# Kernel optimization log

Measured on AMD Instinct MI355X. Metric: run time of the kernel, lower is better.

## Reference

```python
import jax, jax.numpy as jnp
import numpy as np

B, L, D = 16, 1024, 1024
OUT_LEN = 24
N_LAYERS = 3
CYCLE = L
LN_EPS = 1e-5


def _make_pe(seq_len, hidden, cycle):
    # pe[t, j] = 2*pi*t/cycle, then sin on even cols, cos on odd cols
    t = jnp.arange(seq_len, dtype=jnp.float32)[:, None]
    base = (2.0 * jnp.pi * t / cycle) * jnp.ones((1, hidden), jnp.float32)
    cols = jnp.arange(hidden)
    return jnp.where((cols % 2 == 0)[None, :], jnp.sin(base), jnp.cos(base))


def setup_inputs() -> dict:
    key = jax.random.key(0)
    ks = jax.random.split(key, 12)
    s = 0.02
    return {
        "x": jax.random.normal(ks[0], (B, L, D), jnp.float32),
        "pe": _make_pe(L, D, CYCLE),
        "w1": jax.random.normal(ks[1], (N_LAYERS, D, D), jnp.float32) * s,
        "b1": jnp.zeros((N_LAYERS, D), jnp.float32),
        "w2": jax.random.normal(ks[2], (N_LAYERS, D, D), jnp.float32) * s,
        "b2": jnp.zeros((N_LAYERS, D), jnp.float32),
        "ln_g": jnp.ones((N_LAYERS, D), jnp.float32),
        "ln_b": jnp.zeros((N_LAYERS, D), jnp.float32),
        "fc_w": jax.random.normal(ks[3], (1, D), jnp.float32) * s,
        "fc_b": jnp.zeros((1,), jnp.float32),
        "final_w": jax.random.normal(ks[4], (OUT_LEN, L), jnp.float32) * s,
        "final_b": jnp.zeros((OUT_LEN,), jnp.float32),
    }


def _layer_norm(y, g, b):
    mu = jnp.mean(y, axis=-1, keepdims=True)
    var = jnp.mean((y - mu) ** 2, axis=-1, keepdims=True)
    return (y - mu) * jax.lax.rsqrt(var + LN_EPS) * g + b


def reference(x, pe, w1, b1, w2, b2, ln_g, ln_b, fc_w, fc_b, final_w, final_b):
    d = x.shape[-1]
    scale = 1.0 / jnp.sqrt(jnp.float32(d))
    # positional add (pe[:, :seq_len]; here L == D so this is the full buffer)
    h = x + pe[:, : x.shape[1]]
    attns = []
    for l in range(w1.shape[0]):
        # hand-rolled bmm-softmax-bmm self-attention (q = k = v = h)
        scores = jnp.einsum("bqd,bkd->bqk", h, h) * scale  # (B, L, L)
        a = jax.nn.softmax(scores, axis=-1)
        ctx = jnp.einsum("bqk,bkd->bqd", a, h)
        # position-wise FFN with hidden == D, residual over ctx, then LN
        ff = jnp.maximum(ctx @ w1[l].T + b1[l], 0.0) @ w2[l].T + b2[l]
        h = _layer_norm(ctx + ff, ln_g[l], ln_b[l])
        attns.append(a)
    # final head: D -> 1, squeeze, then L -> OUT_LEN over the sequence dim
    z = (h @ fc_w.T + fc_b)[..., 0]  # (B, L)
    out = z @ final_w.T + final_b    # (B, OUT_LEN)
    return (out, jnp.stack(attns))
```

## Files before the change

kernel.cpp:

```cpp
#include <hip/hip_runtime.h>

typedef unsigned short u16;
typedef __attribute__((ext_vector_type(8))) short short8;
typedef __attribute__((ext_vector_type(4))) float f32x4;
typedef __attribute__((ext_vector_type(4))) unsigned short u16x4;

__device__ __forceinline__ float bf2f(u16 u){
  union { unsigned int i; float f; } x; x.i = ((unsigned int)u) << 16; return x.f;
}
__device__ __forceinline__ u16 f2bf(float f){
  union { float f; unsigned int i; } x; x.f = f;
  return (u16)((x.i + 0x7fffu + ((x.i >> 16) & 1u)) >> 16);
}
__device__ __forceinline__ void async16(const void* g, void* s){
  __builtin_amdgcn_global_load_lds((const __attribute__((address_space(1))) void*)g,
                                   (__attribute__((address_space(3))) void*)s, 16, 0, 0);
}

__global__ __launch_bounds__(256) void k_split2(const float* __restrict__ s1, u16* __restrict__ d1,
                                                const float* __restrict__ s2, u16* __restrict__ d2){
  long i = ((long)blockIdx.x * 256 + threadIdx.x) * 4;
  f32x4 v1 = *(const f32x4*)(s1 + i);
  f32x4 v2 = *(const f32x4*)(s2 + i);
  u16x4 h1, h2;
  #pragma unroll
  for (int j=0;j<4;j++){ h1[j] = f2bf(v1[j]); h2[j] = f2bf(v2[j]); }
  *(u16x4*)(d1+i) = h1;
  *(u16x4*)(d2+i) = h2;
}

__global__ __launch_bounds__(256) void k_addpe(const float* __restrict__ x, const float* __restrict__ pe,
                                               u16* __restrict__ d){
  long i = ((long)blockIdx.x * 256 + threadIdx.x) * 4;
  f32x4 xv = *(const f32x4*)(x + i);
  f32x4 pv = *(const f32x4*)(pe + (i & 1048575));
  u16x4 hh;
  #pragma unroll
  for (int j=0;j<4;j++) hh[j] = f2bf(xv[j]+pv[j]);
  *(u16x4*)(d+i) = hh;
}

__global__ __launch_bounds__(256) void k_transpose(const u16* __restrict__ in, u16* __restrict__ outp){
  __shared__ u16 tile[64][68];
  const long b = blockIdx.z;
  const int d0 = blockIdx.x * 64, l0 = blockIdx.y * 64;
  const long ibase = b * 1048576l;
  const int t = threadIdx.x;
  const int cr = t >> 4;
  const int cc = (t & 15) * 4;
  #pragma unroll
  for (int rr=0; rr<4; rr++){
    int row = cr + rr*16;
    u16x4 v = *(const u16x4*)(in + ibase + (long)(l0+row)*1024 + d0 + cc);
    *(u16x4*)&tile[row][cc] = v;
  }
  __syncthreads();
  #pragma unroll
  for (int rr=0; rr<4; rr++){
    int drow = cr + rr*16;
    u16x4 y;
    y[0] = tile[cc+0][drow];
    y[1] = tile[cc+1][drow];
    y[2] = tile[cc+2][drow];
    y[3] = tile[cc+3][drow];
    *(u16x4*)(outp + ibase + (long)(d0+drow)*1024 + l0 + cc) = y;
  }
}

__global__ __launch_bounds__(512, 1) void attn_sm(
    const u16* __restrict__ hB, float* __restrict__ probs, u16* __restrict__ pB)
{
  __shared__ __align__(16) u16 sm[65536];
  const int t = threadIdx.x;
  const int w = t >> 6, lane = t & 63;
  const int fr = lane & 15, fs = lane >> 4;

  const int p = blockIdx.x;
  const int id = (p & 7) * 32 + (p >> 3);
  const long bz = id >> 4;
  const int brow = (id & 15) << 6;

  const u16* hb = hB + bz * 1048576l;

  const u16* gsrc[8];
  int gdst[8];
  #pragma unroll
  for (int c=0;c<8;c++){
    int u = c*512 + t;
    int row = u >> 2;
    int slot = (u & 3) ^ ((row >> 1) & 3);
    gsrc[c] = hb + (long)row*1024 + slot*8;
    gdst[c] = c*4096 + w*512;
  }

  int offA[4], offB[8];
  #pragma unroll
  for (int i=0;i<4;i++){
    int x = i*16 + fr;
    offA[i] = (brow + x)*32 + (fs ^ (((brow + x)>>1)&3))*8;
  }
  #pragma unroll
  for (int j=0;j<8;j++){
    int x = w*128 + j*16 + fr;
    offB[j] = x*32 + (fs ^ ((x>>1)&3))*8;
  }

  f32x4 acc[4][8];
  #pragma unroll
  for (int i=0;i<4;i++)
    #pragma unroll
    for (int j=0;j<8;j++) acc[i][j] = (f32x4){0.f,0.f,0.f,0.f};

  #pragma unroll
  for (int c=0;c<8;c++) async16(gsrc[c], sm + gdst[c]);
  asm volatile("s_waitcnt vmcnt(0)" ::: "memory");
  __builtin_amdgcn_s_barrier();
  __builtin_amdgcn_sched_barrier(0);

#define ATT_BODY(BUF)                                                          \
    short8 aF[4], bF[8];                                                       \
    _Pragma("unroll")                                                          \
    for (int i=0;i<4;i++) aF[i] = *(const short8*)((BUF) + offA[i]);           \
    _Pragma("unroll")                                                          \
    for (int j=0;j<8;j++) bF[j] = *(const short8*)((BUF) + offB[j]);           \
    __builtin_amdgcn_s_setprio(1);                                             \
    _Pragma("unroll")                                                          \
    for (int i=0;i<4;i++)                                                      \
      _Pragma("unroll")                                                        \
      for (int j=0;j<8;j++)                                                    \
        acc[i][j] = __builtin_amdgcn_mfma_f32_16x16x32_bf16(aF[i], bF[j], acc[i][j], 0,0,0); \
    __builtin_amdgcn_s_setprio(0);

  for (int kt = 0; kt < 31; ++kt){
    const u16* buf = sm + (kt & 1)*32768;
    u16* stg = sm + ((kt + 1) & 1)*32768;
    const int ko = (kt + 1)*32;
    #pragma unroll
    for (int c=0;c<8;c++) async16(gsrc[c] + ko, stg + gdst[c]);
    ATT_BODY(buf)
    asm volatile("s_waitcnt vmcnt(0)" ::: "memory");
    __builtin_amdgcn_s_barrier();
    __builtin_amdgcn_sched_barrier(0);
  }
  {
    const u16* buf = sm + 32768;
    ATT_BODY(buf)
  }
#undef ATT_BODY

  float* red = (float*)sm;
  const float SC = 0.03125f;

  float mx[4][4];
  #pragma unroll
  for (int i=0;i<4;i++)
    #pragma unroll
    for (int q=0;q<4;q++){
      float m = acc[i][0][q];
      #pragma unroll
      for (int j=1;j<8;j++) m = fmaxf(m, acc[i][j][q]);
      #pragma unroll
      for (int d=1; d<16; d<<=1) m = fmaxf(m, __shfl_xor(m, d));
      mx[i][q] = m;
    }
  if (fr == 0){
    #pragma unroll
    for (int i=0;i<4;i++)
      #pragma unroll
      for (int q=0;q<4;q++) red[(i*16 + fs*4 + q)*8 + w] = mx[i][q];
  }
  __syncthreads();
  float M[4][4];
  #pragma unroll
  for (int i=0;i<4;i++)
    #pragma unroll
    for (int q=0;q<4;q++){
      const int row = i*16 + fs*4 + q;
      f32x4 a = *(const f32x4*)&red[row*8];
      f32x4 b = *(const f32x4*)&red[row*8+4];
      M[i][q] = fmaxf(fmaxf(fmaxf(a[0],a[1]),fmaxf(a[2],a[3])),
                      fmaxf(fmaxf(b[0],b[1]),fmaxf(b[2],b[3])));
    }
  float sum[4][4];
  #pragma unroll
  for (int i=0;i<4;i++)
    #pragma unroll
    for (int q=0;q<4;q++){
      float s = 0.f;
      #pragma unroll
      for (int j=0;j<8;j++){
        float e = expf((acc[i][j][q] - M[i][q]) * SC);
        acc[i][j][q] = e;
        s += e;
      }
      #pragma unroll
      for (int d=1; d<16; d<<=1) s += __shfl_xor(s, d);
      sum[i][q] = s;
    }
  __syncthreads();
  if (fr == 0){
    #pragma unroll
    for (int i=0;i<4;i++)
      #pragma unroll
      for (int q=0;q<4;q++) red[(i*16 + fs*4 + q)*8 + w] = sum[i][q];
  }
  __syncthreads();
  float inv[4][4];
  #pragma unroll
  for (int i=0;i<4;i++)
    #pragma unroll
    for (int q=0;q<4;q++){
      const int row = i*16 + fs*4 + q;
      f32x4 a = *(const f32x4*)&red[row*8];
      f32x4 b = *(const f32x4*)&red[row*8+4];
      inv[i][q] = 1.0f / (a[0]+a[1]+a[2]+a[3]+b[0]+b[1]+b[2]+b[3]);
    }

  const long obase = bz * 1048576l;
  #pragma unroll
  for (int i=0;i<4;i++)
    #pragma unroll
    for (int q=0;q<4;q++){
      const long rbase = obase + (long)(brow + i*16 + fs*4 + q)*1024;
      const float iv = inv[i][q];
      #pragma unroll
      for (int j=0;j<8;j++){
        const int col = w*128 + j*16 + fr;
        const float pv = acc[i][j][q] * iv;
        probs[rbase + col] = pv;
        pB[rbase + col] = f2bf(pv);
      }
    }
}

template<int MODE>
__global__ __launch_bounds__(512, 2) void gemm8(
    const u16* __restrict__ aB, const u16* __restrict__ bB,
    int per, long sA, long sB, long sC,
    int lda, int ldb, int ldc,
    float scale, const float* __restrict__ bias,
    const u16* __restrict__ res,
    float* __restrict__ cF, u16* __restrict__ cB)
{
  __shared__ __align__(16) u16 sm[65536];
  const int t = threadIdx.x;
  const int w = t >> 6, lane = t & 63;
  const int wm = w >> 2, wn = w & 3;
  const int fr = lane & 15, fs = lane >> 4;

  const int p = blockIdx.x;
  const int chunk = gridDim.x >> 3;
  const int id = (p & 7) * chunk + (p >> 3);
  const long bz = id / per;
  const int rem = id % per;
  const int m0 = (rem >> 2) << 8, n0 = (rem & 3) << 8;

  const u16* a = aB + bz * sA;
  const u16* b = bB + bz * sB;

  const int urow = t >> 2;
  const int col8 = ((t & 3) ^ ((t >> 3) & 3)) * 8;
  const u16* gA0 = a + (long)(m0 + urow) * lda + col8;
  const u16* gA1 = a + (long)(m0 + 128 + urow) * lda + col8;
  const u16* gB0 = b + (long)(n0 + urow) * ldb + col8;
  const u16* gB1 = b + (long)(n0 + 128 + urow) * ldb + col8;
  u16* dA0 = sm + (w << 9);
  u16* dA1 = sm + 4096 + (w << 9);
  u16* dB0 = sm + 8192 + (w << 9);
  u16* dB1 = sm + 12288 + (w << 9);

  int offA[8], offB[4];
  #pragma unroll
  for (int i=0;i<8;i++){
    int row = wm*128 + i*16 + fr;
    int sl = fs ^ ((row >> 1) & 3);
    offA[i] = row*32 + sl*8;
  }
  #pragma unroll
  for (int j=0;j<4;j++){
    int row = wn*64 + j*16 + fr;
    int sl = fs ^ ((row >> 1) & 3);
    offB[j] = 8192 + row*32 + sl*8;
  }

  f32x4 acc[8][4];
  #pragma unroll
  for (int i=0;i<8;i++)
    #pragma unroll
    for (int j=0;j<4;j++) acc[i][j] = (f32x4){0.f,0.f,0.f,0.f};

  #pragma unroll
  for (int pb=0; pb<3; ++pb){
    const int kb = pb*32, sb = pb*16384;
    async16(gA0+kb, dA0+sb); async16(gA1+kb, dA1+sb);
    async16(gB0+kb, dB0+sb); async16(gB1+kb, dB1+sb);
  }
  gA0 += 96; gA1 += 96; gB0 += 96; gB1 += 96;
  asm volatile("s_waitcnt vmcnt(8)" ::: "memory");
  __builtin_amdgcn_s_barrier();
  __builtin_amdgcn_sched_barrier(0);

#define KT_BODY(SMB)                                                           \
    short8 aF[8], bF[4];                                                       \
    _Pragma("unroll")                                                          \
    for (int i=0;i<8;i++) aF[i] = *(const short8*)((SMB) + offA[i]);           \
    _Pragma("unroll")                                                          \
    for (int j=0;j<4;j++) bF[j] = *(const short8*)((SMB) + offB[j]);           \
    __builtin_amdgcn_s_barrier();                                              \
    __builtin_amdgcn_sched_barrier(0);                                         \
    __builtin_amdgcn_s_setprio(1);                                             \
    _Pragma("unroll")                                                          \
    for (int i=0;i<8;i++){                                                     \
      acc[i][0] = __builtin_amdgcn_mfma_f32_16x16x32_bf16(aF[i], bF[0], acc[i][0], 0,0,0); \
      acc[i][1] = __builtin_amdgcn_mfma_f32_16x16x32_bf16(aF[i], bF[1], acc[i][1], 0,0,0); \
    }                                                                          \
    _Pragma("unroll")                                                          \
    for (int i=0;i<8;i++){                                                     \
      acc[i][2] = __builtin_amdgcn_mfma_f32_16x16x32_bf16(aF[i], bF[2], acc[i][2], 0,0,0); \
      acc[i][3] = __builtin_amdgcn_mfma_f32_16x16x32_bf16(aF[i], bF[3], acc[i][3], 0,0,0); \
    }                                                                          \
    __builtin_amdgcn_s_setprio(0);

  for (int kt = 0; kt < 29; ++kt){
    const u16* smb = sm + (kt & 3)*16384;
    const int sb = ((kt + 3) & 3)*16384;
    async16(gA0, dA0+sb); async16(gA1, dA1+sb);
    async16(gB0, dB0+sb); async16(gB1, dB1+sb);
    gA0 += 32; gA1 += 32; gB0 += 32; gB1 += 32;
    KT_BODY(smb)
    asm volatile("s_waitcnt vmcnt(8)" ::: "memory");
    __builtin_amdgcn_s_barrier();
    __builtin_amdgcn_sched_barrier(0);
  }
  {
    const u16* smb = sm + (29 & 3)*16384;
    KT_BODY(smb)
    asm volatile("s_waitcnt vmcnt(4)" ::: "memory");
    __builtin_amdgcn_s_barrier();
    __builtin_amdgcn_sched_barrier(0);
  }
  {
    const u16* smb = sm + (30 & 3)*16384;
    KT_BODY(smb)
    asm volatile("s_waitcnt vmcnt(0)" ::: "memory");
    __builtin_amdgcn_s_barrier();
    __builtin_amdgcn_sched_barrier(0);
  }
  {
    const u16* smb = sm + (31 & 3)*16384;
    KT_BODY(smb)
  }
#undef KT_BODY

  const long cBase = bz * sC;
  const int rb = m0 + wm*128 + fs*4;
  const int cb = n0 + wn*64 + fr;
  #pragma unroll
  for (int j=0;j<4;j++){
    const int c = cb + j*16;
    float bv = 0.f;
    if constexpr (MODE == 2 || MODE == 3) bv = bias[c];
    #pragma unroll
    for (int i=0;i<8;i++){
      #pragma unroll
      for (int q=0;q<4;q++){
        const int r = rb + i*16 + q;
        const long idx = cBase + (long)r*ldc + c;
        float v = acc[i][j][q];
        if constexpr (MODE == 1){
          cB[idx] = f2bf(v);
        } else if constexpr (MODE == 2){
          cB[idx] = f2bf(fmaxf(v + bv, 0.f));
        } else {
          cF[idx] = v + bv + bf2f(res[idx]);
        }
      }
    }
  }
}

__global__ __launch_bounds__(256) void k_ln(const float* __restrict__ r,
                                            const float* __restrict__ g, const float* __restrict__ b,
                                            u16* __restrict__ h){
  const long row = blockIdx.x;
  const float* rr = r + row * 1024;
  const int t = threadIdx.x, w = t >> 6, lane = t & 63;
  __shared__ float rA[4], rB[4];
  f32x4 v = *(const f32x4*)(rr + t*4);
  float s = v[0]+v[1]+v[2]+v[3];
  #pragma unroll
  for (int off=32; off; off>>=1) s += __shfl_xor(s, off);
  if (lane==0) rA[w] = s;
  __syncthreads();
  const float mu = (rA[0]+rA[1]+rA[2]+rA[3]) * (1.0f/1024.0f);
  float sq = 0.f;
  #pragma unroll
  for (int j=0;j<4;j++){ float d = v[j]-mu; sq += d*d; }
  #pragma unroll
  for (int off=32; off; off>>=1) sq += __shfl_xor(sq, off);
  if (lane==0) rB[w] = sq;
  __syncthreads();
  const float var = (rB[0]+rB[1]+rB[2]+rB[3]) * (1.0f/1024.0f);
  const float inv = rsqrtf(var + 1e-5f);
  u16x4 hh;
  #pragma unroll
  for (int j=0;j<4;j++){
    int d = t*4+j;
    hh[j] = f2bf((v[j]-mu)*inv*g[d] + b[d]);
  }
  *(u16x4*)(h + row*1024 + t*4) = hh;
}

__global__ __launch_bounds__(256) void k_final1(const u16* __restrict__ h,
                                                const float* __restrict__ fw, const float* __restrict__ fb,
                                                float* __restrict__ z){
  const int row = blockIdx.x*4 + (threadIdx.x>>6);
  const int lane = threadIdx.x & 63;
  const long base = (long)row * 1024;
  const int d0 = lane * 16;
  float s = 0.f;
  #pragma unroll
  for (int j=0;j<16;j++){
    int d = d0 + j;
    s += bf2f(h[base+d]) * fw[d];
  }
  #pragma unroll
  for (int off=32; off; off>>=1) s += __shfl_xor(s, off);
  if (lane==0) z[row] = s + fb[0];
}

__global__ __launch_bounds__(256) void k_final2(const float* __restrict__ z,
                                                const float* __restrict__ fw, const float* __restrict__ fb,
                                                float* __restrict__ out){
  const int idx = blockIdx.x*4 + (threadIdx.x>>6);
  const int lane = threadIdx.x & 63;
  const int b = idx / 24, o = idx % 24;
  float s = 0.f;
  #pragma unroll
  for (int j=0;j<16;j++){
    int li = lane + j*64;
    s += z[b*1024 + li] * fw[o*1024 + li];
  }
  #pragma unroll
  for (int off=32; off; off>>=1) s += __shfl_xor(s, off);
  if (lane==0) out[idx] = s + fb[o];
}

extern "C" void kernel_launch(void* const* d_in, const int* in_sizes, int n_in,
                              void* d_out, int out_size, void* d_ws, size_t ws_size,
                              hipStream_t stream){
  const float* x   = (const float*)d_in[0];
  const float* pe  = (const float*)d_in[1];
  const float* w1  = (const float*)d_in[2];
  const float* b1  = (const float*)d_in[3];
  const float* w2  = (const float*)d_in[4];
  const float* b2  = (const float*)d_in[5];
  const float* lng = (const float*)d_in[6];
  const float* lnb = (const float*)d_in[7];
  const float* fcw = (const float*)d_in[8];
  const float* fcb = (const float*)d_in[9];
  const float* fw  = (const float*)d_in[10];
  const float* fb  = (const float*)d_in[11];
  float* out  = (float*)d_out;
  float* attn = out + 384;

  char* ws = (char*)d_ws;
  const long BB = 32l*1024*1024;
  u16* hB = (u16*)(ws + 0*BB);
  u16* tB = (u16*)(ws + 1*BB);
  u16* cB = (u16*)(ws + 2*BB);
  u16* pB = (u16*)(ws + 3*BB);
  float* rf = (float*)(ws + 4*BB);
  u16* w1B = (u16*)(ws + 6*BB);
  u16* w2B = w1B + 3l*1024*1024;
  float* z = (float*)(w2B + 3l*1024*1024);

  const long M1 = 1024l*1024;

  k_split2<<<3072, 256, 0, stream>>>(w1, w1B, w2, w2B);
  k_addpe<<<16384, 256, 0, stream>>>(x, pe, hB);
  k_transpose<<<dim3(16,16,16), 256, 0, stream>>>(hB, tB);

  for (int l = 0; l < 3; l++){
    float* sc = attn + (long)l*16*M1;
    attn_sm<<<256, 512, 0, stream>>>(hB, sc, pB);
    gemm8<1><<<256, 512, 0, stream>>>(pB, tB, 16, M1,M1,M1, 1024,1024,1024,
        1.f, nullptr, nullptr, nullptr, cB);
    gemm8<2><<<256, 512, 0, stream>>>(cB, w1B+l*M1, 256, 0,0,0, 1024,1024,1024,
        1.f, b1+l*1024, nullptr, nullptr, pB);
    gemm8<3><<<256, 512, 0, stream>>>(pB, w2B+l*M1, 256, 0,0,0, 1024,1024,1024,
        1.f, b2+l*1024, cB, rf, nullptr);
    k_ln<<<16384, 256, 0, stream>>>(rf, lng+l*1024, lnb+l*1024, hB);
    if (l < 2) k_transpose<<<dim3(16,16,16), 256, 0, stream>>>(hB, tB);
  }

  k_final1<<<4096, 256, 0, stream>>>(hB, fcw, fcb, z);
  k_final2<<<96, 256, 0, stream>>>(z, fw, fb, out);
}
```

Measured before the change: 737.7 us.

## Replace LDS-staged async pipelines with direct global-to-register MFMA fragment loads

Result: slower. 1.543 ms (+109.2%).

```diff
diff --git a/kernel.cpp b/kernel.cpp
--- a/kernel.cpp
+++ b/kernel.cpp
@@ -11,10 +11,6 @@
 __device__ __forceinline__ u16 f2bf(float f){
   union { float f; unsigned int i; } x; x.f = f;
   return (u16)((x.i + 0x7fffu + ((x.i >> 16) & 1u)) >> 16);
-}
-__device__ __forceinline__ void async16(const void* g, void* s){
-  __builtin_amdgcn_global_load_lds((const __attribute__((address_space(1))) void*)g,
-                                   (__attribute__((address_space(3))) void*)s, 16, 0, 0);
 }
 
 __global__ __launch_bounds__(256) void k_split2(const float* __restrict__ s1, u16* __restrict__ d1,
@@ -67,10 +63,10 @@
   }
 }
 
-__global__ __launch_bounds__(512, 1) void attn_sm(
+__global__ __launch_bounds__(512) void attn_sm(
     const u16* __restrict__ hB, float* __restrict__ probs, u16* __restrict__ pB)
 {
-  __shared__ __align__(16) u16 sm[65536];
+  __shared__ float red[512];
   const int t = threadIdx.x;
   const int w = t >> 6, lane = t & 63;
   const int fr = lane & 15, fs = lane >> 4;
@@ -82,28 +78,11 @@
 
   const u16* hb = hB + bz * 1048576l;
 
-  const u16* gsrc[8];
-  int gdst[8];
-  #pragma unroll
-  for (int c=0;c<8;c++){
-    int u = c*512 + t;
-    int row = u >> 2;
-    int slot = (u & 3) ^ ((row >> 1) & 3);
-    gsrc[c] = hb + (long)row*1024 + slot*8;
-    gdst[c] = c*4096 + w*512;
-  }
-
-  int offA[4], offB[8];
-  #pragma unroll
-  for (int i=0;i<4;i++){
-    int x = i*16 + fr;
-    offA[i] = (brow + x)*32 + (fs ^ (((brow + x)>>1)&3))*8;
-  }
-  #pragma unroll
-  for (int j=0;j<8;j++){
-    int x = w*128 + j*16 + fr;
-    offB[j] = x*32 + (fs ^ ((x>>1)&3))*8;
-  }
+  const u16* ga[4]; const u16* gb[8];
+  #pragma unroll
+  for (int i=0;i<4;i++) ga[i] = hb + (long)(brow + i*16 + fr)*1024 + fs*8;
+  #pragma unroll
+  for (int j=0;j<8;j++) gb[j] = hb + (long)(w*128 + j*16 + fr)*1024 + fs*8;
 
   f32x4 acc[4][8];
   #pragma unroll
@@ -111,44 +90,23 @@
     #pragma unroll
     for (int j=0;j<8;j++) acc[i][j] = (f32x4){0.f,0.f,0.f,0.f};
 
-  #pragma unroll
-  for (int c=0;c<8;c++) async16(gsrc[c], sm + gdst[c]);
-  asm volatile("s_waitcnt vmcnt(0)" ::: "memory");
-  __builtin_amdgcn_s_barrier();
-  __builtin_amdgcn_sched_barrier(0);
-
-#define ATT_BODY(BUF)                                                          \
-    short8 aF[4], bF[8];                                                       \
-    _Pragma("unroll")                                                          \
-    for (int i=0;i<4;i++) aF[i] = *(const short8*)((BUF) + offA[i]);           \
-    _Pragma("unroll")                                                          \
-    for (int j=0;j<8;j++) bF[j] = *(const short8*)((BUF) + offB[j]);           \
-    __builtin_amdgcn_s_setprio(1);                                             \
-    _Pragma("unroll")                                                          \
-    for (int i=0;i<4;i++)                                                      \
-      _Pragma("unroll")                                                        \
-      for (int j=0;j<8;j++)                                                    \
-        acc[i][j] = __builtin_amdgcn_mfma_f32_16x16x32_bf16(aF[i], bF[j], acc[i][j], 0,0,0); \
+  #pragma unroll 2
+  for (int kt = 0; kt < 32; ++kt){
+    const int ko = kt*32;
+    short8 aF[4], bF[8];
+    #pragma unroll
+    for (int i=0;i<4;i++) aF[i] = *(const short8*)(ga[i] + ko);
+    #pragma unroll
+    for (int j=0;j<8;j++) bF[j] = *(const short8*)(gb[j] + ko);
+    __builtin_amdgcn_s_setprio(1);
+    #pragma unroll
+    for (int i=0;i<4;i++)
+      #pragma unroll
+      for (int j=0;j<8;j++)
+        acc[i][j] = __builtin_amdgcn_mfma_f32_16x16x32_bf16(aF[i], bF[j], acc[i][j], 0,0,0);
     __builtin_amdgcn_s_setprio(0);
-
-  for (int kt = 0; kt < 31; ++kt){
-    const u16* buf = sm + (kt & 1)*32768;
-    u16* stg = sm + ((kt + 1) & 1)*32768;
-    const int ko = (kt + 1)*32;
-    #pragma unroll
-    for (int c=0;c<8;c++) async16(gsrc[c] + ko, stg + gdst[c]);
-    ATT_BODY(buf)
-    asm volatile("s_waitcnt vmcnt(0)" ::: "memory");
-    __builtin_amdgcn_s_barrier();
-    __builtin_amdgcn_sched_barrier(0);
-  }
-  {
-    const u16* buf = sm + 32768;
-    ATT_BODY(buf)
-  }
-#undef ATT_BODY
-
-  float* red = (float*)sm;
+  }
+
   const float SC = 0.03125f;
 
   float mx[4][4];
@@ -234,18 +192,15 @@
 }
 
 template<int MODE>
-__global__ __launch_bounds__(512, 2) void gemm8(
+__global__ __launch_bounds__(256, 3) void gemmd(
     const u16* __restrict__ aB, const u16* __restrict__ bB,
-    int per, long sA, long sB, long sC,
-    int lda, int ldb, int ldc,
-    float scale, const float* __restrict__ bias,
-    const u16* __restrict__ res,
+    int per, int gridN, long sA, long sB, long sC,
+    const float* __restrict__ bias, const u16* __restrict__ res,
     float* __restrict__ cF, u16* __restrict__ cB)
 {
-  __shared__ __align__(16) u16 sm[65536];
   const int t = threadIdx.x;
   const int w = t >> 6, lane = t & 63;
-  const int wm = w >> 2, wn = w & 3;
+  const int wm = w >> 1, wn = w & 1;
   const int fr = lane & 15, fs = lane >> 4;
 
   const int p = blockIdx.x;
@@ -253,107 +208,42 @@
   const int id = (p & 7) * chunk + (p >> 3);
   const long bz = id / per;
   const int rem = id % per;
-  const int m0 = (rem >> 2) << 8, n0 = (rem & 3) << 8;
+  const int m0 = (rem / gridN) << 7, n0 = (rem % gridN) << 7;
 
   const u16* a = aB + bz * sA;
   const u16* b = bB + bz * sB;
 
-  const int urow = t >> 2;
-  const int col8 = ((t & 3) ^ ((t >> 3) & 3)) * 8;
-  const u16* gA0 = a + (long)(m0 + urow) * lda + col8;
-  const u16* gA1 = a + (long)(m0 + 128 + urow) * lda + col8;
-  const u16* gB0 = b + (long)(n0 + urow) * ldb + col8;
-  const u16* gB1 = b + (long)(n0 + 128 + urow) * ldb + col8;
-  u16* dA0 = sm + (w << 9);
-  u16* dA1 = sm + 4096 + (w << 9);
-  u16* dB0 = sm + 8192 + (w << 9);
-  u16* dB1 = sm + 12288 + (w << 9);
-
-  int offA[8], offB[4];
-  #pragma unroll
-  for (int i=0;i<8;i++){
-    int row = wm*128 + i*16 + fr;
-    int sl = fs ^ ((row >> 1) & 3);
-    offA[i] = row*32 + sl*8;
-  }
-  #pragma unroll
-  for (int j=0;j<4;j++){
-    int row = wn*64 + j*16 + fr;
-    int sl = fs ^ ((row >> 1) & 3);
-    offB[j] = 8192 + row*32 + sl*8;
-  }
-
-  f32x4 acc[8][4];
-  #pragma unroll
-  for (int i=0;i<8;i++)
+  const u16* ga[4]; const u16* gb[4];
+  #pragma unroll
+  for (int i=0;i<4;i++) ga[i] = a + (long)(m0 + wm*64 + i*16 + fr)*1024 + fs*8;
+  #pragma unroll
+  for (int j=0;j<4;j++) gb[j] = b + (long)(n0 + wn*64 + j*16 + fr)*1024 + fs*8;
+
+  f32x4 acc[4][4];
+  #pragma unroll
+  for (int i=0;i<4;i++)
     #pragma unroll
     for (int j=0;j<4;j++) acc[i][j] = (f32x4){0.f,0.f,0.f,0.f};
 
-  #pragma unroll
-  for (int pb=0; pb<3; ++pb){
-    const int kb = pb*32, sb = pb*16384;
-    async16(gA0+kb, dA0+sb); async16(gA1+kb, dA1+sb);
-    async16(gB0+kb, dB0+sb); async16(gB1+kb, dB1+sb);
-  }
-  gA0 += 96; gA1 += 96; gB0 += 96; gB1 += 96;
-  asm volatile("s_waitcnt vmcnt(8)" ::: "memory");
-  __builtin_amdgcn_s_barrier();
-  __builtin_amdgcn_sched_barrier(0);
-
-#define KT_BODY(SMB)                                                           \
-    short8 aF[8], bF[4];                                                       \
-    _Pragma("unroll")                                                          \
-    for (int i=0;i<8;i++) aF[i] = *(const short8*)((SMB) + offA[i]);           \
-    _Pragma("unroll")                                                          \
-    for (int j=0;j<4;j++) bF[j] = *(const short8*)((SMB) + offB[j]);           \
-    __builtin_amdgcn_s_barrier();                                              \
-    __builtin_amdgcn_sched_barrier(0);                                         \
-    __builtin_amdgcn_s_setprio(1);                                             \
-    _Pragma("unroll")                                                          \
-    for (int i=0;i<8;i++){                                                     \
-      acc[i][0] = __builtin_amdgcn_mfma_f32_16x16x32_bf16(aF[i], bF[0], acc[i][0], 0,0,0); \
-      acc[i][1] = __builtin_amdgcn_mfma_f32_16x16x32_bf16(aF[i], bF[1], acc[i][1], 0,0,0); \
-    }                                                                          \
-    _Pragma("unroll")                                                          \
-    for (int i=0;i<8;i++){                                                     \
-      acc[i][2] = __builtin_amdgcn_mfma_f32_16x16x32_bf16(aF[i], bF[2], acc[i][2], 0,0,0); \
-      acc[i][3] = __builtin_amdgcn_mfma_f32_16x16x32_bf16(aF[i], bF[3], acc[i][3], 0,0,0); \
-    }                                                                          \
+  #pragma unroll 2
+  for (int kt = 0; kt < 32; ++kt){
+    const int ko = kt*32;
+    short8 aF[4], bF[4];
+    #pragma unroll
+    for (int i=0;i<4;i++) aF[i] = *(const short8*)(ga[i] + ko);
+    #pragma unroll
+    for (int j=0;j<4;j++) bF[j] = *(const short8*)(gb[j] + ko);
+    __builtin_amdgcn_s_setprio(1);
+    #pragma unroll
+    for (int j=0;j<4;j++)
+      #pragma unroll
+      for (int i=0;i<4;i++)
+        acc[i][j] = __builtin_amdgcn_mfma_f32_16x16x32_bf16(aF[i], bF[j], acc[i][j], 0,0,0);
     __builtin_amdgcn_s_setprio(0);
-
-  for (int kt = 0; kt < 29; ++kt){
-    const u16* smb = sm + (kt & 3)*16384;
-    const int sb = ((kt + 3) & 3)*16384;
-    async16(gA0, dA0+sb); async16(gA1, dA1+sb);
-    async16(gB0, dB0+sb); async16(gB1, dB1+sb);
-    gA0 += 32; gA1 += 32; gB0 += 32; gB1 += 32;
-    KT_BODY(smb)
-    asm volatile("s_waitcnt vmcnt(8)" ::: "memory");
-    __builtin_amdgcn_s_barrier();
-    __builtin_amdgcn_sched_barrier(0);
-  }
-  {
-    const u16* smb = sm + (29 & 3)*16384;
-    KT_BODY(smb)
-    asm volatile("s_waitcnt vmcnt(4)" ::: "memory");
-    __builtin_amdgcn_s_barrier();
-    __builtin_amdgcn_sched_barrier(0);
-  }
-  {
-    const u16* smb = sm + (30 & 3)*16384;
-    KT_BODY(smb)
-    asm volatile("s_waitcnt vmcnt(0)" ::: "memory");
-    __builtin_amdgcn_s_barrier();
-    __builtin_amdgcn_sched_barrier(0);
-  }
-  {
-    const u16* smb = sm + (31 & 3)*16384;
-    KT_BODY(smb)
-  }
-#undef KT_BODY
+  }
 
   const long cBase = bz * sC;
-  const int rb = m0 + wm*128 + fs*4;
+  const int rb = m0 + wm*64 + fs*4;
   const int cb = n0 + wn*64 + fr;
   #pragma unroll
   for (int j=0;j<4;j++){
@@ -361,11 +251,11 @@
     float bv = 0.f;
     if constexpr (MODE == 2 || MODE == 3) bv = bias[c];
     #pragma unroll
-    for (int i=0;i<8;i++){
+    for (int i=0;i<4;i++){
       #pragma unroll
       for (int q=0;q<4;q++){
         const int r = rb + i*16 + q;
-        const long idx = cBase + (long)r*ldc + c;
+        const long idx = cBase + (long)r*1024 + c;
         float v = acc[i][j][q];
         if constexpr (MODE == 1){
           cB[idx] = f2bf(v);
@@ -484,12 +374,12 @@
   for (int l = 0; l < 3; l++){
     float* sc = attn + (long)l*16*M1;
     attn_sm<<<256, 512, 0, stream>>>(hB, sc, pB);
-    gemm8<1><<<256, 512, 0, stream>>>(pB, tB, 16, M1,M1,M1, 1024,1024,1024,
-        1.f, nullptr, nullptr, nullptr, cB);
-    gemm8<2><<<256, 512, 0, stream>>>(cB, w1B+l*M1, 256, 0,0,0, 1024,1024,1024,
-        1.f, b1+l*1024, nullptr, nullptr, pB);
-    gemm8<3><<<256, 512, 0, stream>>>(pB, w2B+l*M1, 256, 0,0,0, 1024,1024,1024,
-        1.f, b2+l*1024, cB, rf, nullptr);
+    gemmd<1><<<1024, 256, 0, stream>>>(pB, tB, 64, 8, M1, M1, M1,
+        nullptr, nullptr, nullptr, cB);
+    gemmd<2><<<1024, 256, 0, stream>>>(cB, w1B+l*M1, 1024, 8, 0, 0, 0,
+        b1+l*1024, nullptr, nullptr, pB);
+    gemmd<3><<<1024, 256, 0, stream>>>(pB, w2B+l*M1, 1024, 8, 0, 0, 0,
+        b2+l*1024, cB, rf, nullptr);
     k_ln<<<16384, 256, 0, stream>>>(rf, lng+l*1024, lnb+l*1024, hB);
     if (l < 2) k_transpose<<<dim3(16,16,16), 256, 0, stream>>>(hB, tB);
   }
```

## Retile GEMMs to 128x256 with 4 waves, 3-stage LDS pipeline, bf16 residual output

Applied to the files above, without the earlier changes.

Result: slower. 800.7 us (+8.5%).

```diff
diff --git a/kernel.cpp b/kernel.cpp
--- a/kernel.cpp
+++ b/kernel.cpp
@@ -234,18 +234,15 @@
 }
 
 template<int MODE>
-__global__ __launch_bounds__(512, 2) void gemm8(
+__global__ __launch_bounds__(256, 2) void gemmh(
     const u16* __restrict__ aB, const u16* __restrict__ bB,
-    int per, long sA, long sB, long sC,
-    int lda, int ldb, int ldc,
-    float scale, const float* __restrict__ bias,
-    const u16* __restrict__ res,
-    float* __restrict__ cF, u16* __restrict__ cB)
+    int per, int gridN, long sA, long sB, long sC,
+    const float* __restrict__ bias, const u16* __restrict__ res,
+    u16* __restrict__ cB)
 {
-  __shared__ __align__(16) u16 sm[65536];
+  __shared__ __align__(16) u16 sm[36864];
   const int t = threadIdx.x;
   const int w = t >> 6, lane = t & 63;
-  const int wm = w >> 2, wn = w & 3;
   const int fr = lane & 15, fs = lane >> 4;
 
   const int p = blockIdx.x;
@@ -253,34 +250,36 @@
   const int id = (p & 7) * chunk + (p >> 3);
   const long bz = id / per;
   const int rem = id % per;
-  const int m0 = (rem >> 2) << 8, n0 = (rem & 3) << 8;
+  const int m0 = (rem / gridN) << 7, n0 = (rem % gridN) << 8;
 
   const u16* a = aB + bz * sA;
   const u16* b = bB + bz * sB;
 
   const int urow = t >> 2;
   const int col8 = ((t & 3) ^ ((t >> 3) & 3)) * 8;
-  const u16* gA0 = a + (long)(m0 + urow) * lda + col8;
-  const u16* gA1 = a + (long)(m0 + 128 + urow) * lda + col8;
-  const u16* gB0 = b + (long)(n0 + urow) * ldb + col8;
-  const u16* gB1 = b + (long)(n0 + 128 + urow) * ldb + col8;
-  u16* dA0 = sm + (w << 9);
-  u16* dA1 = sm + 4096 + (w << 9);
-  u16* dB0 = sm + 8192 + (w << 9);
-  u16* dB1 = sm + 12288 + (w << 9);
+  const u16* gA0 = a + (long)(m0 + urow) * 1024 + col8;
+  const u16* gA1 = a + (long)(m0 + 64 + urow) * 1024 + col8;
+  const u16* gB0 = b + (long)(n0 + urow) * 1024 + col8;
+  const u16* gB1 = b + (long)(n0 + 64 + urow) * 1024 + col8;
+  const u16* gB2 = b + (long)(n0 + 128 + urow) * 1024 + col8;
+  const u16* gB3 = b + (long)(n0 + 192 + urow) * 1024 + col8;
+  const int dA0 = (w << 9);
+  const int dA1 = 2048 + (w << 9);
+  const int dB0 = 4096 + (w << 9);
+  const int dB1 = 6144 + (w << 9);
+  const int dB2 = 8192 + (w << 9);
+  const int dB3 = 10240 + (w << 9);
 
   int offA[8], offB[4];
   #pragma unroll
   for (int i=0;i<8;i++){
-    int row = wm*128 + i*16 + fr;
-    int sl = fs ^ ((row >> 1) & 3);
-    offA[i] = row*32 + sl*8;
+    int row = i*16 + fr;
+    offA[i] = row*32 + (fs ^ ((row >> 1) & 3))*8;
   }
   #pragma unroll
   for (int j=0;j<4;j++){
-    int row = wn*64 + j*16 + fr;
-    int sl = fs ^ ((row >> 1) & 3);
-    offB[j] = 8192 + row*32 + sl*8;
+    int row = w*64 + j*16 + fr;
+    offB[j] = 4096 + row*32 + (fs ^ ((row >> 1) & 3))*8;
   }
 
   f32x4 acc[8][4];
@@ -290,13 +289,14 @@
     for (int j=0;j<4;j++) acc[i][j] = (f32x4){0.f,0.f,0.f,0.f};
 
   #pragma unroll
-  for (int pb=0; pb<3; ++pb){
-    const int kb = pb*32, sb = pb*16384;
-    async16(gA0+kb, dA0+sb); async16(gA1+kb, dA1+sb);
-    async16(gB0+kb, dB0+sb); async16(gB1+kb, dB1+sb);
-  }
-  gA0 += 96; gA1 += 96; gB0 += 96; gB1 += 96;
-  asm volatile("s_waitcnt vmcnt(8)" ::: "memory");
+  for (int pb=0; pb<2; ++pb){
+    const int kb = pb*32, sb = pb*12288;
+    async16(gA0+kb, sm+sb+dA0); async16(gA1+kb, sm+sb+dA1);
+    async16(gB0+kb, sm+sb+dB0); async16(gB1+kb, sm+sb+dB1);
+    async16(gB2+kb, sm+sb+dB2); async16(gB3+kb, sm+sb+dB3);
+  }
+  gA0 += 64; gA1 += 64; gB0 += 64; gB1 += 64; gB2 += 64; gB3 += 64;
+  asm volatile("s_waitcnt vmcnt(6)" ::: "memory");
   __builtin_amdgcn_s_barrier();
   __builtin_amdgcn_sched_barrier(0);
 
@@ -306,55 +306,42 @@
     for (int i=0;i<8;i++) aF[i] = *(const short8*)((SMB) + offA[i]);           \
     _Pragma("unroll")                                                          \
     for (int j=0;j<4;j++) bF[j] = *(const short8*)((SMB) + offB[j]);           \
-    __builtin_amdgcn_s_barrier();                                              \
-    __builtin_amdgcn_sched_barrier(0);                                         \
     __builtin_amdgcn_s_setprio(1);                                             \
     _Pragma("unroll")                                                          \
-    for (int i=0;i<8;i++){                                                     \
-      acc[i][0] = __builtin_amdgcn_mfma_f32_16x16x32_bf16(aF[i], bF[0], acc[i][0], 0,0,0); \
-      acc[i][1] = __builtin_amdgcn_mfma_f32_16x16x32_bf16(aF[i], bF[1], acc[i][1], 0,0,0); \
-    }                                                                          \
-    _Pragma("unroll")                                                          \
-    for (int i=0;i<8;i++){                                                     \
-      acc[i][2] = __builtin_amdgcn_mfma_f32_16x16x32_bf16(aF[i], bF[2], acc[i][2], 0,0,0); \
-      acc[i][3] = __builtin_amdgcn_mfma_f32_16x16x32_bf16(aF[i], bF[3], acc[i][3], 0,0,0); \
-    }                                                                          \
+    for (int j=0;j<4;j++)                                                      \
+      _Pragma("unroll")                                                        \
+      for (int i=0;i<8;i++)                                                    \
+        acc[i][j] = __builtin_amdgcn_mfma_f32_16x16x32_bf16(aF[i], bF[j], acc[i][j], 0,0,0); \
     __builtin_amdgcn_s_setprio(0);
 
-  for (int kt = 0; kt < 29; ++kt){
-    const u16* smb = sm + (kt & 3)*16384;
-    const int sb = ((kt + 3) & 3)*16384;
-    async16(gA0, dA0+sb); async16(gA1, dA1+sb);
-    async16(gB0, dB0+sb); async16(gB1, dB1+sb);
-    gA0 += 32; gA1 += 32; gB0 += 32; gB1 += 32;
+  for (int kt = 0; kt < 30; ++kt){
+    const u16* smb = sm + (kt % 3)*12288;
+    const int sb = ((kt + 2) % 3)*12288;
+    async16(gA0, sm+sb+dA0); async16(gA1, sm+sb+dA1);
+    async16(gB0, sm+sb+dB0); async16(gB1, sm+sb+dB1);
+    async16(gB2, sm+sb+dB2); async16(gB3, sm+sb+dB3);
+    gA0 += 32; gA1 += 32; gB0 += 32; gB1 += 32; gB2 += 32; gB3 += 32;
     KT_BODY(smb)
-    asm volatile("s_waitcnt vmcnt(8)" ::: "memory");
+    asm volatile("s_waitcnt vmcnt(6)" ::: "memory");
     __builtin_amdgcn_s_barrier();
     __builtin_amdgcn_sched_barrier(0);
   }
   {
-    const u16* smb = sm + (29 & 3)*16384;
-    KT_BODY(smb)
-    asm volatile("s_waitcnt vmcnt(4)" ::: "memory");
-    __builtin_amdgcn_s_barrier();
-    __builtin_amdgcn_sched_barrier(0);
-  }
-  {
-    const u16* smb = sm + (30 & 3)*16384;
+    const u16* smb = sm + (30 % 3)*12288;
     KT_BODY(smb)
     asm volatile("s_waitcnt vmcnt(0)" ::: "memory");
     __builtin_amdgcn_s_barrier();
     __builtin_amdgcn_sched_barrier(0);
   }
   {
-    const u16* smb = sm + (31 & 3)*16384;
+    const u16* smb = sm + (31 % 3)*12288;
     KT_BODY(smb)
   }
 #undef KT_BODY
 
   const long cBase = bz * sC;
-  const int rb = m0 + wm*128 + fs*4;
-  const int cb = n0 + wn*64 + fr;
+  const int rb = m0 + fs*4;
+  const int cb = n0 + w*64 + fr;
   #pragma unroll
   for (int j=0;j<4;j++){
     const int c = cb + j*16;
@@ -365,28 +352,31 @@
       #pragma unroll
       for (int q=0;q<4;q++){
         const int r = rb + i*16 + q;
-        const long idx = cBase + (long)r*ldc + c;
+        const long idx = cBase + (long)r*1024 + c;
         float v = acc[i][j][q];
         if constexpr (MODE == 1){
           cB[idx] = f2bf(v);
         } else if constexpr (MODE == 2){
           cB[idx] = f2bf(fmaxf(v + bv, 0.f));
         } else {
-          cF[idx] = v + bv + bf2f(res[idx]);
+          cB[idx] = f2bf(v + bv + bf2f(res[idx]));
         }
       }
     }
   }
 }
 
-__global__ __launch_bounds__(256) void k_ln(const float* __restrict__ r,
+__global__ __launch_bounds__(256) void k_ln(const u16* __restrict__ r,
                                             const float* __restrict__ g, const float* __restrict__ b,
                                             u16* __restrict__ h){
   const long row = blockIdx.x;
-  const float* rr = r + row * 1024;
+  const u16* rr = r + row * 1024;
   const int t = threadIdx.x, w = t >> 6, lane = t & 63;
   __shared__ float rA[4], rB[4];
-  f32x4 v = *(const f32x4*)(rr + t*4);
+  u16x4 rv = *(const u16x4*)(rr + t*4);
+  f32x4 v;
+  #pragma unroll
+  for (int j=0;j<4;j++) v[j] = bf2f(rv[j]);
   float s = v[0]+v[1]+v[2]+v[3];
   #pragma unroll
   for (int off=32; off; off>>=1) s += __shfl_xor(s, off);
@@ -470,7 +460,7 @@
   u16* tB = (u16*)(ws + 1*BB);
   u16* cB = (u16*)(ws + 2*BB);
   u16* pB = (u16*)(ws + 3*BB);
-  float* rf = (float*)(ws + 4*BB);
+  u16* rfB = (u16*)(ws + 4*BB);
   u16* w1B = (u16*)(ws + 6*BB);
   u16* w2B = w1B + 3l*1024*1024;
   float* z = (float*)(w2B + 3l*1024*1024);
@@ -484,13 +474,13 @@
   for (int l = 0; l < 3; l++){
     float* sc = attn + (long)l*16*M1;
     attn_sm<<<256, 512, 0, stream>>>(hB, sc, pB);
-    gemm8<1><<<256, 512, 0, stream>>>(pB, tB, 16, M1,M1,M1, 1024,1024,1024,
-        1.f, nullptr, nullptr, nullptr, cB);
-    gemm8<2><<<256, 512, 0, stream>>>(cB, w1B+l*M1, 256, 0,0,0, 1024,1024,1024,
-        1.f, b1+l*1024, nullptr, nullptr, pB);
-    gemm8<3><<<256, 512, 0, stream>>>(pB, w2B+l*M1, 256, 0,0,0, 1024,1024,1024,
-        1.f, b2+l*1024, cB, rf, nullptr);
-    k_ln<<<16384, 256, 0, stream>>>(rf, lng+l*1024, lnb+l*1024, hB);
+    gemmh<1><<<512, 256, 0, stream>>>(pB, tB, 32, 4, M1, M1, M1,
+        nullptr, nullptr, cB);
+    gemmh<2><<<512, 256, 0, stream>>>(cB, w1B+l*M1, 512, 4, 0, 0, 0,
+        b1+l*1024, nullptr, pB);
+    gemmh<3><<<512, 256, 0, stream>>>(pB, w2B+l*M1, 512, 4, 0, 0, 0,
+        b2+l*1024, cB, rfB);
+    k_ln<<<16384, 256, 0, stream>>>(rfB, lng+l*1024, lnb+l*1024, hB);
     if (l < 2) k_transpose<<<dim3(16,16,16), 256, 0, stream>>>(hB, tB);
   }
 
```
